# Optimization experiments

Hardware: AMD Instinct MI355X
Metric: run time of the kernel (lower is better)

The kernel has to match this reference:

```python
import jax, jax.numpy as jnp
import numpy as np

THRESHOLD = 1.0


def _cif(x, x_len, prob, tgt_len, threshold=THRESHOLD):
    # x: [B,T,D], x_len: [B] int, prob: [B,T], tgt_len: [B] int
    B, T, D = x.shape
    mask = jnp.arange(T)[None, :] < x_len[:, None]           # [B,T]
    prob = prob * mask.astype(prob.dtype)
    tgt = tgt_len.astype(prob.dtype)
    # quantity loss uses UN-normalized prob (matches torch order of ops)
    quantity_loss = jnp.abs(prob.sum(1) - tgt).mean()
    # normalize so masked prob sums to tgt_len (denominator differentiable)
    prob = prob * (tgt / prob.sum(1))[:, None]
    # cum_prob[:,1:] in torch indexing (leading zero implicit via *_prev pads)
    C = jnp.cumsum(prob, axis=1)                             # [B,T]
    Dq = jax.lax.stop_gradient(jnp.floor(C / threshold) * threshold)  # dis_prob (detached)
    C_prev = jnp.pad(C[:, :-1], ((0, 0), (1, 0)))
    D_prev = jnp.pad(Dq[:, :-1], ((0, 0), (1, 0)))
    fire = (Dq != D_prev) & mask                             # firing frames [B,T]
    fire_i = fire.astype(jnp.int32)
    # segment id of each frame's main (pre-fire) weight = #fires strictly before it
    seg = jnp.cumsum(fire_i, axis=1) - fire_i                # [B,T]
    out_len = fire_i.sum(1)                                  # segments emitted per batch
    # weight split per frame: firing frame contributes (Dq - C_prev) to its segment
    # (last_weight) and leftover (C - Dq) to the next segment (remained_weight);
    # non-firing frame contributes its full prob to its segment.
    w_main = jnp.where(fire, Dq - C_prev, prob)              # -> seg
    w_left = jnp.where(fire, C - Dq, jnp.zeros((), prob.dtype))  # -> seg+1
    S = T + 1  # scratch so seg+1 never clips into a valid slot

    def scatter_one(xb, segb, wm, wl, f0):
        out = jnp.zeros((S, xb.shape[-1]), xb.dtype)
        out = out.at[segb].add(wm[:, None] * xb)
        out = out.at[segb + 1].add(wl[:, None] * xb)
        # faithful quirk of the original loop: if frame 0 fires, its leftover is
        # ALSO added to segment 0 (prev_t-1 == t_1-1 there).
        out = out.at[0].add(jnp.where(f0, wl[0], jnp.zeros((), xb.dtype)) * xb[0])
        return out

    out = jax.vmap(scatter_one)(x, seg, w_main, w_left, fire[:, 0])  # [B,S,D]
    out = out[:, :T]
    # drop trailing (never-fired) partial segment contributions, like pad_sequence
    valid = (jnp.arange(T)[None, :] < out_len[:, None]).astype(out.dtype)
    out = out * valid[:, :, None]
    return out, out_len, quantity_loss


def setup_inputs() -> dict:
    key = jax.random.key(0)
    k1, k2, k3, k4 = jax.random.split(key, 4)
    B, T, D = 16, 2048, 512
    x = jax.random.normal(k1, (B, T, D), dtype=jnp.float32)
    x_len = jax.random.randint(k2, (B,), T // 2, T + 1)
    prob = jax.random.uniform(k3, (B, T), dtype=jnp.float32)
    tgt_len = jax.random.randint(k4, (B,), T // 8, T // 4)
    return {"x": x, "x_len": x_len, "prob": prob, "tgt_len": tgt_len}


def reference(x, x_len, prob, tgt_len):
    return _cif(x, x_len, prob, tgt_len)
```

## Files before the change

kernel.cpp:

```cpp
#include <hip/hip_runtime.h>
#include <hip/hip_bf16.h>


constexpr int Bc = 16;
constexpr int Tc = 2048;
constexpr int Dc = 512;
constexpr int SMAX = 512;

typedef float f4 __attribute__((ext_vector_type(4)));

constexpr int ZBLK = 240;
constexpr int ZN   = Bc * (Tc - SMAX) * (Dc / 4);

__global__ __launch_bounds__(256) void cif_scan_kernel(
    const float* __restrict__ prob, const int* __restrict__ x_len,
    const int* __restrict__ tgt_len, float* __restrict__ wm,
    float* __restrict__ wl, int* __restrict__ seg_end,
    int* __restrict__ out_len, double* __restrict__ qloss,
    f4* __restrict__ out4)
{
    const int tid = threadIdx.x;

    if (blockIdx.x >= Bc) {
        const f4 z = {0.f, 0.f, 0.f, 0.f};
        const int idx0   = (blockIdx.x - Bc) * 256 + tid;
        const int stride = ZBLK * 256;
        constexpr int perBatch   = (Tc - SMAX) * (Dc / 4);
        constexpr int batchStrd  = Tc * (Dc / 4);
        constexpr int skip       = SMAX * (Dc / 4);
        for (int j = idx0; j < ZN; j += stride) {
            int b   = j / perBatch;
            int off = j - b * perBatch;
            __builtin_nontemporal_store(z, &out4[(size_t)b * batchStrd + skip + off]);
        }
        return;
    }

    const int b    = blockIdx.x;
    const int lane = tid & 63;
    const int wave = tid >> 6;
    const int xl   = x_len[b];
    const double tgt = (double)tgt_len[b];

    __shared__ double s_wave[4];
    __shared__ double s_bcast;
    __shared__ int    s_wavei[4];

    double p[8];
    double lsum = 0.0;
    const int t0 = tid * 8;
    #pragma unroll
    for (int i = 0; i < 8; ++i) {
        int t = t0 + i;
        float pv = prob[b * Tc + t];
        double v = (t < xl) ? (double)pv : 0.0;
        p[i] = v;
        lsum += v;
    }

    double wsum = lsum;
    #pragma unroll
    for (int off = 32; off > 0; off >>= 1) wsum += __shfl_down(wsum, off, 64);
    if (lane == 0) s_wave[wave] = wsum;
    __syncthreads();
    if (tid == 0) {
        double total = s_wave[0] + s_wave[1] + s_wave[2] + s_wave[3];
        s_bcast = total;
        qloss[b] = fabs(total - tgt);
    }
    __syncthreads();
    const double total = s_bcast;
    const double scale = tgt / total;

    double c[8];
    double run = 0.0;
    #pragma unroll
    for (int i = 0; i < 8; ++i) { p[i] *= scale; run += p[i]; c[i] = run; }

    double xs = run;
    #pragma unroll
    for (int off = 1; off < 64; off <<= 1) {
        double y = __shfl_up(xs, off, 64);
        if (lane >= off) xs += y;
    }
    __syncthreads();
    if (lane == 63) s_wave[wave] = xs;
    __syncthreads();
    double woff = 0.0;
    #pragma unroll
    for (int w = 0; w < 4; ++w) if (w < wave) woff += s_wave[w];
    const double excl = woff + (xs - run);

    int    fire[8];
    double wmv[8], wlv[8];
    int fcnt = 0;
    double Cprev = excl;
    #pragma unroll
    for (int i = 0; i < 8; ++i) {
        int t = t0 + i;
        double C  = excl + c[i];
        double Dq = floor(C);
        double Dp = floor(Cprev);
        bool f = (Dq != Dp) && (t < xl);
        fire[i] = f ? 1 : 0;
        fcnt += fire[i];
        wmv[i] = f ? (Dq - Cprev) : p[i];
        wlv[i] = f ? (C - Dq) : 0.0;
        Cprev = C;
    }

    int fx = fcnt;
    #pragma unroll
    for (int off = 1; off < 64; off <<= 1) {
        int y = __shfl_up(fx, off, 64);
        if (lane >= off) fx += y;
    }
    if (lane == 63) s_wavei[wave] = fx;
    __syncthreads();
    int ioff = 0;
    #pragma unroll
    for (int w = 0; w < 4; ++w) if (w < wave) ioff += s_wavei[w];
    int k = ioff + (fx - fcnt);
    if (tid == 255) out_len[b] = ioff + fx;

    #pragma unroll
    for (int i = 0; i < 8; ++i) {
        int t = t0 + i;
        wm[b * Tc + t] = (float)wmv[i];
        wl[b * Tc + t] = (float)wlv[i];
        if (fire[i]) { seg_end[b * Tc + k] = t; ++k; }
    }
}

__global__ __launch_bounds__(128) void cif_gather_kernel(
    const f4* __restrict__ x4, const float* __restrict__ wm,
    const float* __restrict__ wl, const int* __restrict__ seg_end,
    const int* __restrict__ out_len, const double* __restrict__ qloss,
    f4* __restrict__ out4, float* __restrict__ out_tail)
{
    const int s    = blockIdx.x;
    const int b    = blockIdx.y;
    const int tid  = threadIdx.x;
    const int base = b * Tc;
    const int rs   = Dc / 4;

    f4 acc = {0.f, 0.f, 0.f, 0.f};
    const int ol = out_len[b];
    if (s < ol) {
        const int tEnd = seg_end[base + s];
        const int tBeg = (s == 0) ? 0 : (seg_end[base + s - 1] + 1);
        const f4* xr = x4 + (size_t)base * rs;
        for (int t = tBeg; t <= tEnd; ++t) {
            float w = wm[base + t];
            f4 v = xr[(size_t)t * rs + tid];
            acc += w * v;
        }
        int tl = -1;
        if (s > 0)          tl = tBeg - 1;
        else if (tEnd == 0) tl = 0;
        if (tl >= 0) {
            float w = wl[base + tl];
            f4 v = xr[(size_t)tl * rs + tid];
            acc += w * v;
        }
    }
    __builtin_nontemporal_store(acc, &out4[((size_t)(base + s)) * rs + tid]);

    if (s == 0 && b == 0) {
        if (tid < Bc) out_tail[tid] = (float)out_len[tid];
        if (tid == Bc) {
            double q = 0.0;
            #pragma unroll
            for (int i = 0; i < Bc; ++i) q += qloss[i];
            out_tail[Bc] = (float)(q / (double)Bc);
        }
    }
}

extern "C" void kernel_launch(void* const* d_in, const int* in_sizes, int n_in,
                              void* d_out, int out_size, void* d_ws, size_t ws_size,
                              hipStream_t stream) {
    const float* x       = (const float*)d_in[0];
    const int*   x_len   = (const int*)d_in[1];
    const float* prob    = (const float*)d_in[2];
    const int*   tgt_len = (const int*)d_in[3];

    float* out = (float*)d_out;

    char* ws = (char*)d_ws;
    double* qloss  = (double*)ws;
    float*  wm     = (float*)(ws + 128);
    float*  wl     = (float*)(ws + 128 + Bc*Tc*4);
    int*    segend = (int*)  (ws + 128 + 2*Bc*Tc*4);
    int*    olen   = (int*)  (ws + 128 + 3*Bc*Tc*4);

    cif_scan_kernel<<<Bc + ZBLK, 256, 0, stream>>>(prob, x_len, tgt_len,
                                                   wm, wl, segend, olen, qloss,
                                                   (f4*)out);
    cif_gather_kernel<<<dim3(SMAX, Bc), 128, 0, stream>>>(
        (const f4*)x, wm, wl, segend, olen, qloss,
        (f4*)out, out + (size_t)Bc * Tc * Dc);
}
```

Measured before the change: 120.1 us.

## Fuse scan and gather into one cooperative kernel with grid sync

Merges the scan and zero-fill kernel with the segment-gather kernel into a single cooperative launch of 512 blocks, using a grid-wide barrier between phases. The gather phase now gives each wave a whole output row (two f4 per lane) in a grid-stride loop instead of one 128-thread block per row. This removes one kernel launch and its inter-kernel gap. In exchange it adds grid-sync cost, and the gather runs with fewer resident workers than the original 8192-block grid, which may reduce latency hiding.

```diff
diff --git a/kernel.cpp b/kernel.cpp
--- a/kernel.cpp
+++ b/kernel.cpp
@@ -1,172 +1,145 @@
 #include <hip/hip_runtime.h>
 #include <hip/hip_bf16.h>
+#include <hip/hip_cooperative_groups.h>
+
+namespace cg = cooperative_groups;
 
 
 constexpr int Bc = 16;
 constexpr int Tc = 2048;
 constexpr int Dc = 512;
 constexpr int SMAX = 512;
+constexpr int GRID = 512;
 
 typedef float f4 __attribute__((ext_vector_type(4)));
 
-constexpr int ZBLK = 240;
-constexpr int ZN   = Bc * (Tc - SMAX) * (Dc / 4);
-
-__global__ __launch_bounds__(256) void cif_scan_kernel(
+__global__ __launch_bounds__(256) void cif_fused_kernel(
     const float* __restrict__ prob, const int* __restrict__ x_len,
     const int* __restrict__ tgt_len, float* __restrict__ wm,
     float* __restrict__ wl, int* __restrict__ seg_end,
     int* __restrict__ out_len, double* __restrict__ qloss,
-    f4* __restrict__ out4)
+    const f4* __restrict__ x4, f4* __restrict__ out4,
+    float* __restrict__ out_tail)
 {
-    const int tid = threadIdx.x;
-
-    if (blockIdx.x >= Bc) {
+    const int tid  = threadIdx.x;
+    const int blk  = blockIdx.x;
+    const int lane = tid & 63;
+    const int wave = tid >> 6;
+    constexpr int rs = Dc / 4;
+
+    __shared__ double s_wave[4];
+    __shared__ double s_bcast;
+    __shared__ int    s_wavei[4];
+
+    if (blk < Bc) {
+        const int b = blk;
+        const int xl = x_len[b];
+        const double tgt = (double)tgt_len[b];
+
+        double p[8];
+        double lsum = 0.0;
+        const int t0 = tid * 8;
+        #pragma unroll
+        for (int i = 0; i < 8; ++i) {
+            int t = t0 + i;
+            float pv = prob[b * Tc + t];
+            double v = (t < xl) ? (double)pv : 0.0;
+            p[i] = v;
+            lsum += v;
+        }
+
+        double wsum = lsum;
+        #pragma unroll
+        for (int off = 32; off > 0; off >>= 1) wsum += __shfl_down(wsum, off, 64);
+        if (lane == 0) s_wave[wave] = wsum;
+        __syncthreads();
+        if (tid == 0) {
+            double total = s_wave[0] + s_wave[1] + s_wave[2] + s_wave[3];
+            s_bcast = total;
+            qloss[b] = fabs(total - tgt);
+        }
+        __syncthreads();
+        const double total = s_bcast;
+        const double scale = tgt / total;
+
+        double c[8];
+        double run = 0.0;
+        #pragma unroll
+        for (int i = 0; i < 8; ++i) { p[i] *= scale; run += p[i]; c[i] = run; }
+
+        double xs = run;
+        #pragma unroll
+        for (int off = 1; off < 64; off <<= 1) {
+            double y = __shfl_up(xs, off, 64);
+            if (lane >= off) xs += y;
+        }
+        __syncthreads();
+        if (lane == 63) s_wave[wave] = xs;
+        __syncthreads();
+        double woff = 0.0;
+        #pragma unroll
+        for (int w = 0; w < 4; ++w) if (w < wave) woff += s_wave[w];
+        const double excl = woff + (xs - run);
+
+        int    fire[8];
+        double wmv[8], wlv[8];
+        int fcnt = 0;
+        double Cprev = excl;
+        #pragma unroll
+        for (int i = 0; i < 8; ++i) {
+            int t = t0 + i;
+            double C  = excl + c[i];
+            double Dq = floor(C);
+            double Dp = floor(Cprev);
+            bool f = (Dq != Dp) && (t < xl);
+            fire[i] = f ? 1 : 0;
+            fcnt += fire[i];
+            wmv[i] = f ? (Dq - Cprev) : p[i];
+            wlv[i] = f ? (C - Dq) : 0.0;
+            Cprev = C;
+        }
+
+        int fx = fcnt;
+        #pragma unroll
+        for (int off = 1; off < 64; off <<= 1) {
+            int y = __shfl_up(fx, off, 64);
+            if (lane >= off) fx += y;
+        }
+        if (lane == 63) s_wavei[wave] = fx;
+        __syncthreads();
+        int ioff = 0;
+        #pragma unroll
+        for (int w = 0; w < 4; ++w) if (w < wave) ioff += s_wavei[w];
+        int k = ioff + (fx - fcnt);
+        if (tid == 255) out_len[b] = ioff + fx;
+
+        #pragma unroll
+        for (int i = 0; i < 8; ++i) {
+            int t = t0 + i;
+            wm[b * Tc + t] = (float)wmv[i];
+            wl[b * Tc + t] = (float)wlv[i];
+            if (fire[i]) { seg_end[b * Tc + k] = t; ++k; }
+        }
+        __threadfence();
+    } else {
         const f4 z = {0.f, 0.f, 0.f, 0.f};
-        const int idx0   = (blockIdx.x - Bc) * 256 + tid;
-        const int stride = ZBLK * 256;
-        constexpr int perBatch   = (Tc - SMAX) * (Dc / 4);
-        constexpr int batchStrd  = Tc * (Dc / 4);
-        constexpr int skip       = SMAX * (Dc / 4);
+        const int nzb    = (int)gridDim.x - Bc;
+        const int idx0   = (blk - Bc) * 256 + tid;
+        const int stride = nzb * 256;
+        constexpr int perBatch  = (Tc - SMAX) * rs;
+        constexpr int batchStrd = Tc * rs;
+        constexpr int skip      = SMAX * rs;
+        constexpr int ZN        = Bc * perBatch;
         for (int j = idx0; j < ZN; j += stride) {
             int b   = j / perBatch;
             int off = j - b * perBatch;
             __builtin_nontemporal_store(z, &out4[(size_t)b * batchStrd + skip + off]);
         }
-        return;
     }
 
-    const int b    = blockIdx.x;
-    const int lane = tid & 63;
-    const int wave = tid >> 6;
-    const int xl   = x_len[b];
-    const double tgt = (double)tgt_len[b];
-
-    __shared__ double s_wave[4];
-    __shared__ double s_bcast;
-    __shared__ int    s_wavei[4];
-
-    double p[8];
-    double lsum = 0.0;
-    const int t0 = tid * 8;
-    #pragma unroll
-    for (int i = 0; i < 8; ++i) {
-        int t = t0 + i;
-        float pv = prob[b * Tc + t];
-        double v = (t < xl) ? (double)pv : 0.0;
-        p[i] = v;
-        lsum += v;
-    }
-
-    double wsum = lsum;
-    #pragma unroll
-    for (int off = 32; off > 0; off >>= 1) wsum += __shfl_down(wsum, off, 64);
-    if (lane == 0) s_wave[wave] = wsum;
-    __syncthreads();
-    if (tid == 0) {
-        double total = s_wave[0] + s_wave[1] + s_wave[2] + s_wave[3];
-        s_bcast = total;
-        qloss[b] = fabs(total - tgt);
-    }
-    __syncthreads();
-    const double total = s_bcast;
-    const double scale = tgt / total;
-
-    double c[8];
-    double run = 0.0;
-    #pragma unroll
-    for (int i = 0; i < 8; ++i) { p[i] *= scale; run += p[i]; c[i] = run; }
-
-    double xs = run;
-    #pragma unroll
-    for (int off = 1; off < 64; off <<= 1) {
-        double y = __shfl_up(xs, off, 64);
-        if (lane >= off) xs += y;
-    }
-    __syncthreads();
-    if (lane == 63) s_wave[wave] = xs;
-    __syncthreads();
-    double woff = 0.0;
-    #pragma unroll
-    for (int w = 0; w < 4; ++w) if (w < wave) woff += s_wave[w];
-    const double excl = woff + (xs - run);
-
-    int    fire[8];
-    double wmv[8], wlv[8];
-    int fcnt = 0;
-    double Cprev = excl;
-    #pragma unroll
-    for (int i = 0; i < 8; ++i) {
-        int t = t0 + i;
-        double C  = excl + c[i];
-        double Dq = floor(C);
-        double Dp = floor(Cprev);
-        bool f = (Dq != Dp) && (t < xl);
-        fire[i] = f ? 1 : 0;
-        fcnt += fire[i];
-        wmv[i] = f ? (Dq - Cprev) : p[i];
-        wlv[i] = f ? (C - Dq) : 0.0;
-        Cprev = C;
-    }
-
-    int fx = fcnt;
-    #pragma unroll
-    for (int off = 1; off < 64; off <<= 1) {
-        int y = __shfl_up(fx, off, 64);
-        if (lane >= off) fx += y;
-    }
-    if (lane == 63) s_wavei[wave] = fx;
-    __syncthreads();
-    int ioff = 0;
-    #pragma unroll
-    for (int w = 0; w < 4; ++w) if (w < wave) ioff += s_wavei[w];
-    int k = ioff + (fx - fcnt);
-    if (tid == 255) out_len[b] = ioff + fx;
-
-    #pragma unroll
-    for (int i = 0; i < 8; ++i) {
-        int t = t0 + i;
-        wm[b * Tc + t] = (float)wmv[i];
-        wl[b * Tc + t] = (float)wlv[i];
-        if (fire[i]) { seg_end[b * Tc + k] = t; ++k; }
-    }
-}
-
-__global__ __launch_bounds__(128) void cif_gather_kernel(
-    const f4* __restrict__ x4, const float* __restrict__ wm,
-    const float* __restrict__ wl, const int* __restrict__ seg_end,
-    const int* __restrict__ out_len, const double* __restrict__ qloss,
-    f4* __restrict__ out4, float* __restrict__ out_tail)
-{
-    const int s    = blockIdx.x;
-    const int b    = blockIdx.y;
-    const int tid  = threadIdx.x;
-    const int base = b * Tc;
-    const int rs   = Dc / 4;
-
-    f4 acc = {0.f, 0.f, 0.f, 0.f};
-    const int ol = out_len[b];
-    if (s < ol) {
-        const int tEnd = seg_end[base + s];
-        const int tBeg = (s == 0) ? 0 : (seg_end[base + s - 1] + 1);
-        const f4* xr = x4 + (size_t)base * rs;
-        for (int t = tBeg; t <= tEnd; ++t) {
-            float w = wm[base + t];
-            f4 v = xr[(size_t)t * rs + tid];
-            acc += w * v;
-        }
-        int tl = -1;
-        if (s > 0)          tl = tBeg - 1;
-        else if (tEnd == 0) tl = 0;
-        if (tl >= 0) {
-            float w = wl[base + tl];
-            f4 v = xr[(size_t)tl * rs + tid];
-            acc += w * v;
-        }
-    }
-    __builtin_nontemporal_store(acc, &out4[((size_t)(base + s)) * rs + tid]);
-
-    if (s == 0 && b == 0) {
+    cg::this_grid().sync();
+
+    if (blk == 0) {
         if (tid < Bc) out_tail[tid] = (float)out_len[tid];
         if (tid == Bc) {
             double q = 0.0;
@@ -174,6 +147,42 @@
             for (int i = 0; i < Bc; ++i) q += qloss[i];
             out_tail[Bc] = (float)(q / (double)Bc);
         }
+    }
+
+    const int waveId   = blk * 4 + wave;
+    const int totWaves = (int)gridDim.x * 4;
+    const int nRows    = Bc * SMAX;
+    for (int row = waveId; row < nRows; row += totWaves) {
+        const int b    = row >> 9;
+        const int s    = row & (SMAX - 1);
+        const int base = b * Tc;
+
+        f4 a0 = {0.f, 0.f, 0.f, 0.f};
+        f4 a1 = a0;
+        const int ol = out_len[b];
+        if (s < ol) {
+            const int tEnd = seg_end[base + s];
+            const int tBeg = (s == 0) ? 0 : (seg_end[base + s - 1] + 1);
+            const f4* xr = x4 + (size_t)base * rs;
+            for (int t = tBeg; t <= tEnd; ++t) {
+                float w = wm[base + t];
+                const f4* xp = xr + (size_t)t * rs;
+                a0 += w * xp[lane];
+                a1 += w * xp[lane + 64];
+            }
+            int tl = -1;
+            if (s > 0)          tl = tBeg - 1;
+            else if (tEnd == 0) tl = 0;
+            if (tl >= 0) {
+                float w = wl[base + tl];
+                const f4* xp = xr + (size_t)tl * rs;
+                a0 += w * xp[lane];
+                a1 += w * xp[lane + 64];
+            }
+        }
+        f4* op = out4 + (size_t)(base + s) * rs;
+        __builtin_nontemporal_store(a0, &op[lane]);
+        __builtin_nontemporal_store(a1, &op[lane + 64]);
     }
 }
 
@@ -194,10 +203,14 @@
     int*    segend = (int*)  (ws + 128 + 2*Bc*Tc*4);
     int*    olen   = (int*)  (ws + 128 + 3*Bc*Tc*4);
 
-    cif_scan_kernel<<<Bc + ZBLK, 256, 0, stream>>>(prob, x_len, tgt_len,
-                                                   wm, wl, segend, olen, qloss,
-                                                   (f4*)out);
-    cif_gather_kernel<<<dim3(SMAX, Bc), 128, 0, stream>>>(
-        (const f4*)x, wm, wl, segend, olen, qloss,
-        (f4*)out, out + (size_t)Bc * Tc * Dc);
+    const f4* x4       = (const f4*)x;
+    f4*       out4     = (f4*)out;
+    float*    out_tail = out + (size_t)Bc * Tc * Dc;
+
+    void* args[] = { (void*)&prob, (void*)&x_len, (void*)&tgt_len,
+                     (void*)&wm, (void*)&wl, (void*)&segend, (void*)&olen,
+                     (void*)&qloss, (void*)&x4, (void*)&out4, (void*)&out_tail };
+
+    hipLaunchCooperativeKernel((const void*)cif_fused_kernel,
+                               dim3(GRID), dim3(256), args, 0, stream);
 }
```

New measurement: 212.4 us. 76.8% more time.
